# Optimization experiments

Measured on AMD Instinct MI355X. Metric: run time of the kernel, lower is better.

Reference implementation:

```python
import jax, jax.numpy as jnp
import numpy as np
import math

D_IN = 1024
D_OUT = 1024
NUM_HEADS = 16
HEAD_DIM = D_OUT // NUM_HEADS
B = 2
S = 4096


def setup_inputs() -> dict:
    key = jax.random.key(0)
    ks = jax.random.split(key, 6)
    x = jax.random.normal(ks[0], (B, S, D_IN), dtype=jnp.float32)
    # kaiming-uniform-ish scale for weights; exact init values don't matter for correctness
    bound = 1.0 / math.sqrt(D_IN)
    Wq = jax.random.uniform(ks[1], (D_OUT, D_IN), minval=-bound, maxval=bound, dtype=jnp.float32)
    Wk = jax.random.uniform(ks[2], (D_OUT, D_IN), minval=-bound, maxval=bound, dtype=jnp.float32)
    Wv = jax.random.uniform(ks[3], (D_OUT, D_IN), minval=-bound, maxval=bound, dtype=jnp.float32)
    Wo = jax.random.uniform(ks[4], (D_OUT, D_OUT), minval=-bound, maxval=bound, dtype=jnp.float32)
    bo = jax.random.uniform(ks[5], (D_OUT,), minval=-bound, maxval=bound, dtype=jnp.float32)
    return {"x": x, "Wq": Wq, "Wk": Wk, "Wv": Wv, "Wo": Wo, "bo": bo}


@jax.custom_vjp
def binarize(w):
    return jnp.sign(w)

def _bin_fwd(w):
    return jnp.sign(w), w

def _bin_bwd(w, g):
    # straight-through estimator: pass grad where |w| <= 1
    return (g * (jnp.abs(w) <= 1).astype(g.dtype),)

binarize.defvjp(_bin_fwd, _bin_bwd)


def reference(x, Wq, Wk, Wv, Wo, bo):
    b, n, _ = x.shape
    h, hd = NUM_HEADS, HEAD_DIM
    # binarized projections (torch F.linear: x @ W.T)
    q = (x @ binarize(Wq).T).reshape(b, n, h, hd).transpose(0, 2, 1, 3)  # [b,h,n,hd]
    k = (x @ binarize(Wk).T).reshape(b, n, h, hd).transpose(0, 2, 1, 3)
    v = (x @ binarize(Wv).T).reshape(b, n, h, hd).transpose(0, 2, 1, 3)
    scores = jnp.einsum('bhqd,bhkd->bhqk', q, k) / math.sqrt(hd)  # [b,h,n,n]
    causal = jnp.tril(jnp.ones((n, n), dtype=bool))
    scores = jnp.where(causal, scores, -jnp.inf)
    attn = jax.nn.softmax(scores, axis=-1)
    # dropout p=0.0 -> identity
    ctx = jnp.einsum('bhqk,bhkd->bqhd', attn, v).reshape(b, n, h * hd)
    return ctx @ binarize(Wo).T + bo
```

## Files before the change

### kernel.cpp

```cpp
#include <hip/hip_runtime.h>
#include <hip/hip_bf16.h>
#include <cstdint>
#include <cstddef>

#define S 4096
#define D 1024
#define H 16
#define HD 64
#define BATCH 2
#define M_TOK 8192
#define K2 2048

typedef short short8 __attribute__((ext_vector_type(8)));
typedef __bf16 bf16x8 __attribute__((ext_vector_type(8)));
typedef float f32x4 __attribute__((ext_vector_type(4)));
typedef unsigned int u32;

static __device__ __forceinline__ ushort f2bf(float f) {
  union { float f; uint32_t u; } v; v.f = f;
  uint32_t u = v.u + 0x7FFFu + ((v.u >> 16) & 1u);
  return (ushort)(u >> 16);
}
static __device__ __forceinline__ float bf2f(ushort h) {
  union { uint32_t u; float f; } v; v.u = ((uint32_t)h) << 16; return v.f;
}
static __device__ __forceinline__ uint32_t cvtpk(float lo, float hi) {
  uint32_t r;
  asm("v_cvt_pk_bf16_f32 %0, %1, %2" : "=v"(r) : "v"(lo), "v"(hi));
  return r;
}
static __device__ __forceinline__ float vexp2(float x) {
  float r;
  asm("v_exp_f32 %0, %1" : "=v"(r) : "v"(x));
  return r;
}
static __device__ __forceinline__ bf16x8 pack4(uint32_t a, uint32_t b, uint32_t c, uint32_t d) {
  union { uint32_t u[4]; bf16x8 v; } z;
  z.u[0] = a; z.u[1] = b; z.u[2] = c; z.u[3] = d;
  return z.v;
}
static __device__ __forceinline__ void gld16(const void* g, void* l) {
  __builtin_amdgcn_global_load_lds(
      (const __attribute__((address_space(1))) u32*)g,
      (__attribute__((address_space(3))) u32*)l, 16, 0, 0);
}
static __device__ __forceinline__ ushort sgn(float a) {
  return a > 0.f ? 0x3F80 : (a < 0.f ? 0xBF80 : 0);
}

__global__ void prep_x(const float* __restrict__ x, ushort* __restrict__ xcat) {
  int i = blockIdx.x * blockDim.x + threadIdx.x;
  const int total = M_TOK * 128;
  for (; i < total; i += gridDim.x * blockDim.x) {
    int row = i >> 7, c8 = (i & 127) * 8;
    const float* px = &x[(size_t)row * 1024 + c8];
    float4 a = *(const float4*)px;
    float4 b = *(const float4*)(px + 4);
    float va[8] = {a.x, a.y, a.z, a.w, b.x, b.y, b.z, b.w};
    union { ushort u[8]; short8 v; } Hh, Ll;
#pragma unroll
    for (int j = 0; j < 8; ++j) {
      ushort h = f2bf(va[j]);
      Hh.u[j] = h;
      Ll.u[j] = f2bf(va[j] - bf2f(h));
    }
    *(short8*)&xcat[(size_t)row * K2 + c8] = Hh.v;
    *(short8*)&xcat[(size_t)row * K2 + 1024 + c8] = Ll.v;
  }
}

__global__ void prep_w(const float* __restrict__ wq, const float* __restrict__ wk,
                       const float* __restrict__ wv, const float* __restrict__ wo,
                       ushort* __restrict__ wcat, ushort* __restrict__ wob) {
  int i = blockIdx.x * blockDim.x + threadIdx.x;
  const int total = (D * D) / 4;
  for (; i < total; i += gridDim.x * blockDim.x) {
    float4 a;
    union { ushort u[4]; uint2 v; } t;
    a = *(const float4*)&wq[i * 4];
    t.u[0] = sgn(a.x); t.u[1] = sgn(a.y); t.u[2] = sgn(a.z); t.u[3] = sgn(a.w);
    *(uint2*)&wcat[i * 4] = t.v;
    a = *(const float4*)&wk[i * 4];
    t.u[0] = sgn(a.x); t.u[1] = sgn(a.y); t.u[2] = sgn(a.z); t.u[3] = sgn(a.w);
    *(uint2*)&wcat[D * D + i * 4] = t.v;
    a = *(const float4*)&wv[i * 4];
    t.u[0] = sgn(a.x); t.u[1] = sgn(a.y); t.u[2] = sgn(a.z); t.u[3] = sgn(a.w);
    *(uint2*)&wcat[2 * D * D + i * 4] = t.v;
    a = *(const float4*)&wo[i * 4];
    t.u[0] = sgn(a.x); t.u[1] = sgn(a.y); t.u[2] = sgn(a.z); t.u[3] = sgn(a.w);
    *(uint2*)&wob[i * 4] = t.v;
  }
}

template<int EPI, int KK, int BROW>
__global__ __launch_bounds__(256) void gemm97(
    const ushort* __restrict__ A, const ushort* __restrict__ Bw,
    ushort* __restrict__ q_hi, ushort* __restrict__ q_lo,
    ushort* __restrict__ k_hi, ushort* __restrict__ k_lo,
    ushort* __restrict__ v_t,
    float* __restrict__ of, const float* __restrict__ bias)
{
  __shared__ ushort smA[128 * 32];
  __shared__ ushort smB[128 * 32];
  const int tid = threadIdx.x;
  const int l = tid & 63;
  const int w = tid >> 6;
  const int x = l & 15, g = l >> 4;
  const int wm = w >> 1, wn = w & 1;
  const int bm = blockIdx.x, bn = blockIdx.y;

  const ushort* gA[2]; const ushort* gB[2]; int ldso[2];
#pragma unroll
  for (int p = 0; p < 2; ++p) {
    int q = p * 256 + tid;
    gA[p] = &A[(size_t)(bm * 128 + (q >> 2)) * KK + (q & 3) * 8];
    gB[p] = &Bw[(size_t)(bn * 128 + (q >> 2)) * BROW + (q & 3) * 8];
    ldso[p] = (p * 256 + w * 64) * 8;
  }

  f32x4 acc[4][4] = {};

  for (int k0 = 0; k0 < KK; k0 += 32) {
    __syncthreads();
#pragma unroll
    for (int p = 0; p < 2; ++p) {
      gld16(gA[p] + k0, &smA[ldso[p]]);
      gld16(gB[p] + (k0 & (BROW - 1)), &smB[ldso[p]]);
    }
    __syncthreads();
    bf16x8 af[4], bf_[4];
#pragma unroll
    for (int m = 0; m < 4; ++m)
      af[m] = *(const bf16x8*)&smA[(wm * 64 + m * 16 + x) * 32 + g * 8];
#pragma unroll
    for (int n = 0; n < 4; ++n)
      bf_[n] = *(const bf16x8*)&smB[(wn * 64 + n * 16 + x) * 32 + g * 8];
#pragma unroll
    for (int m = 0; m < 4; ++m)
#pragma unroll
      for (int n = 0; n < 4; ++n)
        acc[m][n] = __builtin_amdgcn_mfma_f32_16x16x32_bf16(af[m], bf_[n], acc[m][n], 0, 0, 0);
  }

  if (EPI == 0) {
    const int proj = bn >> 3;
    ushort* oh = (proj == 0) ? q_hi : k_hi;
    ushort* ol = (proj == 0) ? q_lo : k_lo;
#pragma unroll
    for (int m = 0; m < 4; ++m)
#pragma unroll
      for (int n = 0; n < 4; ++n)
#pragma unroll
        for (int r = 0; r < 4; ++r) {
          int rowg = bm * 128 + wm * 64 + m * 16 + g * 4 + r;
          int colg = bn * 128 + wn * 64 + n * 16 + x;
          float v = acc[m][n][r];
          int bi = rowg >> 12, ntok = rowg & 4095;
          int cg = colg & 1023;
          int h = cg >> 6, hd = cg & 63;
          size_t bhb = (size_t)(bi * H + h) * (S * HD);
          if (proj < 2) {
            size_t off = bhb + (size_t)ntok * HD + hd;
            ushort hiv = f2bf(v);
            oh[off] = hiv;
            ol[off] = f2bf(v - bf2f(hiv));
          } else {
            int t5 = ntok & 31;
            int pos = ((t5 >> 2) & 3) * 8 + ((t5 >> 4) & 1) * 4 + (t5 & 3);
            v_t[bhb + (size_t)hd * S + (ntok & ~31) + pos] = f2bf(v);
          }
        }
  } else {
#pragma unroll
    for (int m = 0; m < 4; ++m)
#pragma unroll
      for (int n = 0; n < 4; ++n)
#pragma unroll
        for (int r = 0; r < 4; ++r) {
          int rowg = bm * 128 + wm * 64 + m * 16 + g * 4 + r;
          int colg = bn * 128 + wn * 64 + n * 16 + x;
          of[(size_t)rowg * D + colg] = acc[m][n][r] + bias[colg];
        }
  }
}

__global__ __launch_bounds__(256) void flash3(
    const ushort* __restrict__ qhi, const ushort* __restrict__ qlo,
    const ushort* __restrict__ khi, const ushort* __restrict__ klo,
    const ushort* __restrict__ vt, ushort* __restrict__ ctx)
{
  __shared__ ushort smKhi[64 * 64];
  __shared__ ushort smKlo[64 * 64];
  __shared__ ushort smVT[64 * 64];

  const int tid = threadIdx.x;
  const int l = tid & 63;
  const int w = tid >> 6;
  const int x = l & 15;
  const int g = l >> 4;
  const int bh = blockIdx.x;
  const int qt = (int)(gridDim.y - 1) - (int)blockIdx.y;
  const int qbase = qt * 128;
  const size_t qkbase = (size_t)bh * S * HD;

  int soff_k[2]; size_t soff_v[2]; int ldso[2];
#pragma unroll
  for (int p = 0; p < 2; ++p) {
    int q = p * 256 + tid;
    int rr = q >> 3;
    int sb = (q & 7) ^ (rr & 7);
    soff_k[p] = rr * HD + sb * 8;
    soff_v[p] = (size_t)rr * S + sb * 8;
    ldso[p] = (p * 256 + w * 64) * 8;
  }

  bf16x8 bq[2][2][2];
#pragma unroll
  for (int qs = 0; qs < 2; ++qs) {
    int qrow = qbase + w * 32 + qs * 16 + x;
    size_t base = qkbase + (size_t)qrow * HD + g * 8;
    bq[qs][0][0] = *(const bf16x8*)&qhi[base];
    bq[qs][0][1] = *(const bf16x8*)&qhi[base + 32];
    bq[qs][1][0] = *(const bf16x8*)&qlo[base];
    bq[qs][1][1] = *(const bf16x8*)&qlo[base + 32];
  }

  float mrun[2] = {-1e30f, -1e30f};
  float lrun[2] = {0.f, 0.f};
  f32x4 oacc[2][4] = {};

  const int kvmax = (qbase + 127) >> 6;
  const int qmaxw = qbase + w * 32 + 31;
  const float C1 = 0.125f * 1.44269504f;
  const float TH = 8.0f / C1;

  for (int kv = 0; kv <= kvmax; ++kv) {
    const ushort* kh  = khi + qkbase + (size_t)kv * 64 * HD;
    const ushort* klp = klo + qkbase + (size_t)kv * 64 * HD;
    const ushort* vtp = vt  + qkbase + (size_t)kv * 64;
    __syncthreads();
#pragma unroll
    for (int p = 0; p < 2; ++p) {
      gld16(kh + soff_k[p], &smKhi[ldso[p]]);
      gld16(klp + soff_k[p], &smKlo[ldso[p]]);
      gld16(vtp + soff_v[p], &smVT[ldso[p]]);
    }
    __syncthreads();
    if (kv * 64 > qmaxw) continue;

    f32x4 scq[2][4];
    __builtin_amdgcn_s_setprio(1);
#pragma unroll
    for (int t = 0; t < 4; ++t) {
      f32x4 a0 = {}, a1 = {};
#pragma unroll
      for (int c = 0; c < 2; ++c) {
        int pb = (t * 16 + x) * 64 + ((4 * c + g) ^ (x & 7)) * 8;
        bf16x8 kH = *(const bf16x8*)&smKhi[pb];
        bf16x8 kL = *(const bf16x8*)&smKlo[pb];
        a0 = __builtin_amdgcn_mfma_f32_16x16x32_bf16(kH, bq[0][0][c], a0, 0, 0, 0);
        a0 = __builtin_amdgcn_mfma_f32_16x16x32_bf16(kL, bq[0][0][c], a0, 0, 0, 0);
        a0 = __builtin_amdgcn_mfma_f32_16x16x32_bf16(kH, bq[0][1][c], a0, 0, 0, 0);
        a1 = __builtin_amdgcn_mfma_f32_16x16x32_bf16(kH, bq[1][0][c], a1, 0, 0, 0);
        a1 = __builtin_amdgcn_mfma_f32_16x16x32_bf16(kL, bq[1][0][c], a1, 0, 0, 0);
        a1 = __builtin_amdgcn_mfma_f32_16x16x32_bf16(kH, bq[1][1][c], a1, 0, 0, 0);
      }
      scq[0][t] = a0; scq[1][t] = a1;
    }
    __builtin_amdgcn_s_setprio(0);

    const bool needmask = (kv * 64 + 63 > qbase + w * 32);
    uint32_t pbq[2][2][4];

#pragma unroll
    for (int qs = 0; qs < 2; ++qs) {
      if (needmask) {
        int qglob = qbase + w * 32 + qs * 16 + x;
        int kb = kv * 64 + 4 * g;
#pragma unroll
        for (int t = 0; t < 4; ++t)
#pragma unroll
          for (int r = 0; r < 4; ++r)
            if (kb + t * 16 + r > qglob) scq[qs][t][r] = -1e30f;
      }
      float mloc = scq[qs][0][0];
#pragma unroll
      for (int t = 0; t < 4; ++t)
#pragma unroll
        for (int r = 0; r < 4; ++r) mloc = fmaxf(mloc, scq[qs][t][r]);
      mloc = fmaxf(mloc, __shfl_xor(mloc, 16));
      mloc = fmaxf(mloc, __shfl_xor(mloc, 32));
      if (!__all(mloc <= mrun[qs] + TH)) {
        float mnew = fmaxf(mrun[qs], mloc);
        float scal = vexp2((mrun[qs] - mnew) * C1);
        mrun[qs] = mnew;
        lrun[qs] *= scal;
#pragma unroll
        for (int dt = 0; dt < 4; ++dt) oacc[qs][dt] *= scal;
      }
      float mc = mrun[qs] * C1;
      float ps = 0.f;
#pragma unroll
      for (int t = 0; t < 4; ++t)
#pragma unroll
        for (int r = 0; r < 4; ++r) {
          float pv = vexp2(scq[qs][t][r] * C1 - mc);
          scq[qs][t][r] = pv;
          ps += pv;
        }
      ps += __shfl_xor(ps, 16);
      ps += __shfl_xor(ps, 32);
      lrun[qs] += ps;
#pragma unroll
      for (int c = 0; c < 2; ++c) {
        pbq[qs][c][0] = cvtpk(scq[qs][2 * c][0], scq[qs][2 * c][1]);
        pbq[qs][c][1] = cvtpk(scq[qs][2 * c][2], scq[qs][2 * c][3]);
        pbq[qs][c][2] = cvtpk(scq[qs][2 * c + 1][0], scq[qs][2 * c + 1][1]);
        pbq[qs][c][3] = cvtpk(scq[qs][2 * c + 1][2], scq[qs][2 * c + 1][3]);
      }
    }

    __builtin_amdgcn_s_setprio(1);
#pragma unroll
    for (int c = 0; c < 2; ++c)
#pragma unroll
      for (int dt = 0; dt < 4; ++dt) {
        bf16x8 vf = *(const bf16x8*)&smVT[(dt * 16 + x) * 64 + ((4 * c + g) ^ (x & 7)) * 8];
        oacc[0][dt] = __builtin_amdgcn_mfma_f32_16x16x32_bf16(
            vf, pack4(pbq[0][c][0], pbq[0][c][1], pbq[0][c][2], pbq[0][c][3]), oacc[0][dt], 0, 0, 0);
        oacc[1][dt] = __builtin_amdgcn_mfma_f32_16x16x32_bf16(
            vf, pack4(pbq[1][c][0], pbq[1][c][1], pbq[1][c][2], pbq[1][c][3]), oacc[1][dt], 0, 0, 0);
      }
    __builtin_amdgcn_s_setprio(0);
  }

  const int b = bh >> 4, h = bh & 15;
#pragma unroll
  for (int qs = 0; qs < 2; ++qs) {
    float inv = 1.0f / lrun[qs];
    int tok = qbase + w * 32 + qs * 16 + x;
#pragma unroll
    for (int dt = 0; dt < 4; ++dt) {
      uint2 uu;
      uu.x = cvtpk(oacc[qs][dt][0] * inv, oacc[qs][dt][1] * inv);
      uu.y = cvtpk(oacc[qs][dt][2] * inv, oacc[qs][dt][3] * inv);
      *(uint2*)&ctx[(size_t)(b * S + tok) * D + h * 64 + dt * 16 + 4 * g] = uu;
    }
  }
}

extern "C" void kernel_launch(void* const* d_in, const int* in_sizes, int n_in,
                              void* d_out, int out_size, void* d_ws, size_t ws_size,
                              hipStream_t stream) {
  const float* x  = (const float*)d_in[0];
  const float* Wq = (const float*)d_in[1];
  const float* Wk = (const float*)d_in[2];
  const float* Wv = (const float*)d_in[3];
  const float* Wo = (const float*)d_in[4];
  const float* bo = (const float*)d_in[5];
  float* out = (float*)d_out;

  if (ws_size < (size_t)120 * 1024 * 1024) return;

  char* ws = (char*)d_ws;
  const size_t MB = 1024 * 1024;
  ushort* xcat = (ushort*)(ws);
  ushort* ctx  = (ushort*)(ws);
  ushort* wcat = (ushort*)(ws + 32 * MB);
  ushort* wob  = (ushort*)(ws + 38 * MB);
  ushort* qhi  = (ushort*)(ws + 40 * MB);
  ushort* qlo  = (ushort*)(ws + 56 * MB);
  ushort* khi  = (ushort*)(ws + 72 * MB);
  ushort* klo  = (ushort*)(ws + 88 * MB);
  ushort* vt   = (ushort*)(ws + 104 * MB);

  prep_x<<<2048, 256, 0, stream>>>(x, xcat);
  prep_w<<<1024, 256, 0, stream>>>(Wq, Wk, Wv, Wo, wcat, wob);

  gemm97<0, K2, 1024><<<dim3(64, 24), 256, 0, stream>>>(
      xcat, wcat, qhi, qlo, khi, klo, vt, nullptr, nullptr);

  flash3<<<dim3(BATCH * H, S / 128), 256, 0, stream>>>(qhi, qlo, khi, klo, vt, ctx);

  gemm97<2, 1024, 1024><<<dim3(64, 8), 256, 0, stream>>>(
      ctx, wob, nullptr, nullptr, nullptr, nullptr, nullptr, out, bo);
}
```

Before: 339.9 us.

## Double-buffer K/V tiles in flash attention to overlap loads with compute

```diff
diff --git a/kernel.cpp b/kernel.cpp
--- a/kernel.cpp
+++ b/kernel.cpp
@@ -184,14 +184,14 @@
   }
 }
 
-__global__ __launch_bounds__(256) void flash3(
+__global__ __launch_bounds__(256) void flash4(
     const ushort* __restrict__ qhi, const ushort* __restrict__ qlo,
     const ushort* __restrict__ khi, const ushort* __restrict__ klo,
     const ushort* __restrict__ vt, ushort* __restrict__ ctx)
 {
-  __shared__ ushort smKhi[64 * 64];
-  __shared__ ushort smKlo[64 * 64];
-  __shared__ ushort smVT[64 * 64];
+  __shared__ ushort smKhi[2][64 * 64];
+  __shared__ ushort smKlo[2][64 * 64];
+  __shared__ ushort smVT[2][64 * 64];
 
   const int tid = threadIdx.x;
   const int l = tid & 63;
@@ -213,6 +213,9 @@
     soff_v[p] = (size_t)rr * S + sb * 8;
     ldso[p] = (p * 256 + w * 64) * 8;
   }
+  const ushort* khb = khi + qkbase;
+  const ushort* klb = klo + qkbase;
+  const ushort* vtb = vt + qkbase;
 
   bf16x8 bq[2][2][2];
 #pragma unroll
@@ -234,104 +237,124 @@
   const float C1 = 0.125f * 1.44269504f;
   const float TH = 8.0f / C1;
 
+#pragma unroll
+  for (int p = 0; p < 2; ++p) {
+    gld16(khb + soff_k[p], &smKhi[0][ldso[p]]);
+    gld16(klb + soff_k[p], &smKlo[0][ldso[p]]);
+    gld16(vtb + soff_v[p], &smVT[0][ldso[p]]);
+  }
+  __syncthreads();
+
+  int cur = 0;
   for (int kv = 0; kv <= kvmax; ++kv) {
-    const ushort* kh  = khi + qkbase + (size_t)kv * 64 * HD;
-    const ushort* klp = klo + qkbase + (size_t)kv * 64 * HD;
-    const ushort* vtp = vt  + qkbase + (size_t)kv * 64;
-    __syncthreads();
-#pragma unroll
-    for (int p = 0; p < 2; ++p) {
-      gld16(kh + soff_k[p], &smKhi[ldso[p]]);
-      gld16(klp + soff_k[p], &smKlo[ldso[p]]);
-      gld16(vtp + soff_v[p], &smVT[ldso[p]]);
-    }
-    __syncthreads();
-    if (kv * 64 > qmaxw) continue;
-
-    f32x4 scq[2][4];
-    __builtin_amdgcn_s_setprio(1);
-#pragma unroll
-    for (int t = 0; t < 4; ++t) {
-      f32x4 a0 = {}, a1 = {};
-#pragma unroll
-      for (int c = 0; c < 2; ++c) {
-        int pb = (t * 16 + x) * 64 + ((4 * c + g) ^ (x & 7)) * 8;
-        bf16x8 kH = *(const bf16x8*)&smKhi[pb];
-        bf16x8 kL = *(const bf16x8*)&smKlo[pb];
-        a0 = __builtin_amdgcn_mfma_f32_16x16x32_bf16(kH, bq[0][0][c], a0, 0, 0, 0);
-        a0 = __builtin_amdgcn_mfma_f32_16x16x32_bf16(kL, bq[0][0][c], a0, 0, 0, 0);
-        a0 = __builtin_amdgcn_mfma_f32_16x16x32_bf16(kH, bq[0][1][c], a0, 0, 0, 0);
-        a1 = __builtin_amdgcn_mfma_f32_16x16x32_bf16(kH, bq[1][0][c], a1, 0, 0, 0);
-        a1 = __builtin_amdgcn_mfma_f32_16x16x32_bf16(kL, bq[1][0][c], a1, 0, 0, 0);
-        a1 = __builtin_amdgcn_mfma_f32_16x16x32_bf16(kH, bq[1][1][c], a1, 0, 0, 0);
-      }
-      scq[0][t] = a0; scq[1][t] = a1;
-    }
-    __builtin_amdgcn_s_setprio(0);
-
-    const bool needmask = (kv * 64 + 63 > qbase + w * 32);
-    uint32_t pbq[2][2][4];
-
-#pragma unroll
-    for (int qs = 0; qs < 2; ++qs) {
-      if (needmask) {
-        int qglob = qbase + w * 32 + qs * 16 + x;
-        int kb = kv * 64 + 4 * g;
-#pragma unroll
-        for (int t = 0; t < 4; ++t)
-#pragma unroll
-          for (int r = 0; r < 4; ++r)
-            if (kb + t * 16 + r > qglob) scq[qs][t][r] = -1e30f;
-      }
-      float mloc = scq[qs][0][0];
-#pragma unroll
-      for (int t = 0; t < 4; ++t)
-#pragma unroll
-        for (int r = 0; r < 4; ++r) mloc = fmaxf(mloc, scq[qs][t][r]);
-      mloc = fmaxf(mloc, __shfl_xor(mloc, 16));
-      mloc = fmaxf(mloc, __shfl_xor(mloc, 32));
-      if (!__all(mloc <= mrun[qs] + TH)) {
-        float mnew = fmaxf(mrun[qs], mloc);
-        float scal = vexp2((mrun[qs] - mnew) * C1);
-        mrun[qs] = mnew;
-        lrun[qs] *= scal;
-#pragma unroll
-        for (int dt = 0; dt < 4; ++dt) oacc[qs][dt] *= scal;
-      }
-      float mc = mrun[qs] * C1;
-      float ps = 0.f;
-#pragma unroll
-      for (int t = 0; t < 4; ++t)
-#pragma unroll
-        for (int r = 0; r < 4; ++r) {
-          float pv = vexp2(scq[qs][t][r] * C1 - mc);
-          scq[qs][t][r] = pv;
-          ps += pv;
-        }
-      ps += __shfl_xor(ps, 16);
-      ps += __shfl_xor(ps, 32);
-      lrun[qs] += ps;
-#pragma unroll
-      for (int c = 0; c < 2; ++c) {
-        pbq[qs][c][0] = cvtpk(scq[qs][2 * c][0], scq[qs][2 * c][1]);
-        pbq[qs][c][1] = cvtpk(scq[qs][2 * c][2], scq[qs][2 * c][3]);
-        pbq[qs][c][2] = cvtpk(scq[qs][2 * c + 1][0], scq[qs][2 * c + 1][1]);
-        pbq[qs][c][3] = cvtpk(scq[qs][2 * c + 1][2], scq[qs][2 * c + 1][3]);
+    if (kv < kvmax) {
+      const ushort* kh = khb + (size_t)(kv + 1) * (64 * HD);
+      const ushort* kl = klb + (size_t)(kv + 1) * (64 * HD);
+      const ushort* vp = vtb + (size_t)(kv + 1) * 64;
+      int nb = cur ^ 1;
+#pragma unroll
+      for (int p = 0; p < 2; ++p) {
+        gld16(kh + soff_k[p], &smKhi[nb][ldso[p]]);
+        gld16(kl + soff_k[p], &smKlo[nb][ldso[p]]);
+        gld16(vp + soff_v[p], &smVT[nb][ldso[p]]);
       }
     }
 
-    __builtin_amdgcn_s_setprio(1);
-#pragma unroll
-    for (int c = 0; c < 2; ++c)
-#pragma unroll
-      for (int dt = 0; dt < 4; ++dt) {
-        bf16x8 vf = *(const bf16x8*)&smVT[(dt * 16 + x) * 64 + ((4 * c + g) ^ (x & 7)) * 8];
-        oacc[0][dt] = __builtin_amdgcn_mfma_f32_16x16x32_bf16(
-            vf, pack4(pbq[0][c][0], pbq[0][c][1], pbq[0][c][2], pbq[0][c][3]), oacc[0][dt], 0, 0, 0);
-        oacc[1][dt] = __builtin_amdgcn_mfma_f32_16x16x32_bf16(
-            vf, pack4(pbq[1][c][0], pbq[1][c][1], pbq[1][c][2], pbq[1][c][3]), oacc[1][dt], 0, 0, 0);
+    if (kv * 64 <= qmaxw) {
+      const ushort* bKhi = smKhi[cur];
+      const ushort* bKlo = smKlo[cur];
+      const ushort* bVT = smVT[cur];
+
+      f32x4 scq[2][4];
+      __builtin_amdgcn_s_setprio(1);
+#pragma unroll
+      for (int t = 0; t < 4; ++t) {
+        f32x4 a0 = {}, a1 = {};
+#pragma unroll
+        for (int c = 0; c < 2; ++c) {
+          int pb = (t * 16 + x) * 64 + ((4 * c + g) ^ (x & 7)) * 8;
+          bf16x8 kH = *(const bf16x8*)&bKhi[pb];
+          bf16x8 kL = *(const bf16x8*)&bKlo[pb];
+          a0 = __builtin_amdgcn_mfma_f32_16x16x32_bf16(kH, bq[0][0][c], a0, 0, 0, 0);
+          a0 = __builtin_amdgcn_mfma_f32_16x16x32_bf16(kL, bq[0][0][c], a0, 0, 0, 0);
+          a0 = __builtin_amdgcn_mfma_f32_16x16x32_bf16(kH, bq[0][1][c], a0, 0, 0, 0);
+          a1 = __builtin_amdgcn_mfma_f32_16x16x32_bf16(kH, bq[1][0][c], a1, 0, 0, 0);
+          a1 = __builtin_amdgcn_mfma_f32_16x16x32_bf16(kL, bq[1][0][c], a1, 0, 0, 0);
+          a1 = __builtin_amdgcn_mfma_f32_16x16x32_bf16(kH, bq[1][1][c], a1, 0, 0, 0);
+        }
+        scq[0][t] = a0; scq[1][t] = a1;
       }
-    __builtin_amdgcn_s_setprio(0);
+      __builtin_amdgcn_s_setprio(0);
+
+      const bool needmask = (kv * 64 + 63 > qbase + w * 32);
+      uint32_t pbq[2][2][4];
+
+#pragma unroll
+      for (int qs = 0; qs < 2; ++qs) {
+        if (needmask) {
+          int qglob = qbase + w * 32 + qs * 16 + x;
+          int kb = kv * 64 + 4 * g;
+#pragma unroll
+          for (int t = 0; t < 4; ++t)
+#pragma unroll
+            for (int r = 0; r < 4; ++r)
+              if (kb + t * 16 + r > qglob) scq[qs][t][r] = -1e30f;
+        }
+        float mt[4];
+#pragma unroll
+        for (int t = 0; t < 4; ++t)
+          mt[t] = fmaxf(fmaxf(scq[qs][t][0], scq[qs][t][1]),
+                        fmaxf(scq[qs][t][2], scq[qs][t][3]));
+        float mloc = fmaxf(fmaxf(mt[0], mt[1]), fmaxf(mt[2], mt[3]));
+        mloc = fmaxf(mloc, __shfl_xor(mloc, 16));
+        mloc = fmaxf(mloc, __shfl_xor(mloc, 32));
+        if (!__all(mloc <= mrun[qs] + TH)) {
+          float mnew = fmaxf(mrun[qs], mloc);
+          float scal = vexp2((mrun[qs] - mnew) * C1);
+          mrun[qs] = mnew;
+          lrun[qs] *= scal;
+#pragma unroll
+          for (int dt = 0; dt < 4; ++dt) oacc[qs][dt] *= scal;
+        }
+        float mc = mrun[qs] * C1;
+#pragma unroll
+        for (int t = 0; t < 4; ++t)
+#pragma unroll
+          for (int r = 0; r < 4; ++r)
+            scq[qs][t][r] = vexp2(scq[qs][t][r] * C1 - mc);
+        float st[4];
+#pragma unroll
+        for (int t = 0; t < 4; ++t)
+          st[t] = (scq[qs][t][0] + scq[qs][t][1]) + (scq[qs][t][2] + scq[qs][t][3]);
+        float ps = (st[0] + st[1]) + (st[2] + st[3]);
+        ps += __shfl_xor(ps, 16);
+        ps += __shfl_xor(ps, 32);
+        lrun[qs] += ps;
+#pragma unroll
+        for (int c = 0; c < 2; ++c) {
+          pbq[qs][c][0] = cvtpk(scq[qs][2 * c][0], scq[qs][2 * c][1]);
+          pbq[qs][c][1] = cvtpk(scq[qs][2 * c][2], scq[qs][2 * c][3]);
+          pbq[qs][c][2] = cvtpk(scq[qs][2 * c + 1][0], scq[qs][2 * c + 1][1]);
+          pbq[qs][c][3] = cvtpk(scq[qs][2 * c + 1][2], scq[qs][2 * c + 1][3]);
+        }
+      }
+
+      __builtin_amdgcn_s_setprio(1);
+#pragma unroll
+      for (int c = 0; c < 2; ++c)
+#pragma unroll
+        for (int dt = 0; dt < 4; ++dt) {
+          bf16x8 vf = *(const bf16x8*)&bVT[(dt * 16 + x) * 64 + ((4 * c + g) ^ (x & 7)) * 8];
+          oacc[0][dt] = __builtin_amdgcn_mfma_f32_16x16x32_bf16(
+              vf, pack4(pbq[0][c][0], pbq[0][c][1], pbq[0][c][2], pbq[0][c][3]), oacc[0][dt], 0, 0, 0);
+          oacc[1][dt] = __builtin_amdgcn_mfma_f32_16x16x32_bf16(
+              vf, pack4(pbq[1][c][0], pbq[1][c][1], pbq[1][c][2], pbq[1][c][3]), oacc[1][dt], 0, 0, 0);
+        }
+      __builtin_amdgcn_s_setprio(0);
+    }
+
+    __syncthreads();
+    cur ^= 1;
   }
 
   const int b = bh >> 4, h = bh & 15;
@@ -380,7 +403,7 @@
   gemm97<0, K2, 1024><<<dim3(64, 24), 256, 0, stream>>>(
       xcat, wcat, qhi, qlo, khi, klo, vt, nullptr, nullptr);
 
-  flash3<<<dim3(BATCH * H, S / 128), 256, 0, stream>>>(qhi, qlo, khi, klo, vt, ctx);
+  flash4<<<dim3(BATCH * H, S / 128), 256, 0, stream>>>(qhi, qlo, khi, klo, vt, ctx);
 
   gemm97<2, 1024, 1024><<<dim3(64, 8), 256, 0, stream>>>(
       ctx, wob, nullptr, nullptr, nullptr, nullptr, nullptr, out, bo);
```

New measurement: 349.2 us. 2.8% more time.
